# Kernel optimization log

Measured on AMD Instinct MI355X. Metric: run time of the kernel, lower is better.

The kernel has to match this reference:

```python
import jax, jax.numpy as jnp
import numpy as np

N_NODES = 50000
N_EDGES = 500000
D = 128          # n_features
HID = 64         # explainer MLP hidden dim
TEMP = 5.0       # temp[0], epoch-0 temperature
SAMPLE_BIAS = 0.0


def setup_inputs() -> dict:
    key = jax.random.key(0)
    ks = jax.random.split(key, 8)
    embeds = jax.random.normal(ks[0], (N_NODES, D), dtype=jnp.float32)
    W1 = jax.random.normal(ks[1], (3 * D, HID), dtype=jnp.float32) * 0.05
    b1 = jnp.zeros((HID,), dtype=jnp.float32)
    W2 = jax.random.normal(ks[2], (HID, 1), dtype=jnp.float32) * 0.05
    b2 = jnp.zeros((1,), dtype=jnp.float32)
    u = jax.random.uniform(ks[3], (N_EDGES, 1), dtype=jnp.float32)
    src = jax.random.randint(ks[4], (N_EDGES,), 0, N_NODES, dtype=jnp.int64 if jax.config.jax_enable_x64 else jnp.int32)
    dst = jax.random.randint(ks[5], (N_EDGES,), 0, N_NODES, dtype=jnp.int64 if jax.config.jax_enable_x64 else jnp.int32)
    n = 0  # target node index within the subgraph
    return {"embeds": embeds, "W1": W1, "b1": b1, "W2": W2, "b2": b2,
            "u": u, "src": src, "dst": dst, "n": n}


def reference(embeds, W1, b1, W2, b2, u, src, dst, n):
    # --- _create_explainer_input: edge-wise gather + concat with target node embed ---
    row_embeds = embeds[src]                                   # [E, D]
    col_embeds = embeds[dst]                                   # [E, D]
    node_data = jnp.broadcast_to(embeds[n][None, :], row_embeds.shape)  # [E, D]
    inputs = jnp.concatenate([row_embeds, col_embeds, node_data], axis=1)  # [E, 3D]
    # --- explainer_model: Linear(3D,64) -> ReLU -> Linear(64,1) ---
    h = jax.nn.relu(inputs @ W1 + b1)                          # [E, HID]
    sampling_weights = h @ W2 + b2                             # [E, 1]
    # --- _sample_graph (training=True): Gumbel-sigmoid ---
    bias = SAMPLE_BIAS + 0.0001
    eps = (bias - (1.0 - bias)) * u + (1.0 - bias)             # U(bias, 1-bias)
    gate_inputs = jnp.log(eps) - jnp.log1p(-eps)
    mask = jax.nn.sigmoid((gate_inputs + sampling_weights) / TEMP)
    return mask.squeeze(-1)                                    # [E]
```

## Files before the change

### kernel.cpp

```cpp
#include <hip/hip_runtime.h>
#include <hip/hip_bf16.h>


#define D 128
#define HID 64

typedef __attribute__((ext_vector_type(8))) short short8;
typedef __attribute__((ext_vector_type(4))) float f32x4;

__device__ inline unsigned short f2bf(float f) {
    union { float f; unsigned int u; } x;
    x.f = f;
    unsigned int r = x.u + 0x7FFFu + ((x.u >> 16) & 1u);
    return (unsigned short)(r >> 16);
}

__device__ inline unsigned int f2e5u(float f) {
    _Float16 h = (_Float16)f;
    unsigned short u;
    __builtin_memcpy(&u, &h, 2);
    unsigned short r = (unsigned short)(u + 0x7Fu + ((u >> 8) & 1u));
    return (unsigned int)(r >> 8) & 0xFFu;
}
__device__ inline float e5(unsigned short hibits) {
    _Float16 h;
    __builtin_memcpy(&h, &hibits, 2);
    return (float)h;
}

__global__ __launch_bounds__(256) void pg_prep(
    const float* __restrict__ embeds, const float* __restrict__ W1,
    const float* __restrict__ b1, const int* __restrict__ nidx,
    unsigned short* __restrict__ bfrag, float* __restrict__ cnode)
{
    int t = threadIdx.x;
    if (blockIdx.x < 64) {
        int i    = blockIdx.x * 256 + t;
        int j    = i & 7;
        int lane = (i >> 3) & 63;
        int ct   = (i >> 9) & 7;
        int ks   = i >> 12;
        int k    = ks * 32 + (lane >> 4) * 8 + j;
        int col  = ct * 16 + (lane & 15);
        float w  = (col < HID) ? W1[k * HID + col]
                               : W1[(D + k) * HID + (col - HID)];
        bfrag[i] = f2bf(w);
    } else if (t < HID) {
        int n = nidx[0];
        const float* nr = embeds + (size_t)n * D;
        float c = b1[t];
        #pragma unroll 8
        for (int k = 0; k < D; ++k)
            c = fmaf(nr[k], W1[(2 * D + k) * HID + t], c);
        cnode[t] = c;
    }
}

__global__ __launch_bounds__(256) void pg_nodes(
    const float* __restrict__ embeds, const unsigned short* __restrict__ bfrag,
    unsigned char* __restrict__ P, int N, int NTILES)
{
    __shared__ short wl[16384];
    __shared__ unsigned char st[4][16 * 144];
    {
        const uint4* s = reinterpret_cast<const uint4*>(bfrag);
        uint4* d = reinterpret_cast<uint4*>(wl);
        #pragma unroll
        for (int i = 0; i < 8; ++i)
            d[threadIdx.x + i * 256] = s[threadIdx.x + i * 256];
    }
    __syncthreads();

    int wave  = threadIdx.x >> 6;
    int lane  = threadIdx.x & 63;
    int ntile = blockIdx.x * 4 + wave;
    bool active = (ntile < NTILES);

    int kg = lane >> 4;
    if (active) {
        int nr = ntile * 16 + (lane & 15);
        if (nr >= N) nr = N - 1;
        const float* row = embeds + (size_t)nr * D + kg * 8;

        short8 af[4];
        #pragma unroll
        for (int ks = 0; ks < 4; ++ks) {
            float4 v0 = *reinterpret_cast<const float4*>(row + ks * 32);
            float4 v1 = *reinterpret_cast<const float4*>(row + ks * 32 + 4);
            union { float f; unsigned u; } c[8];
            c[0].f = v0.x; c[1].f = v0.y; c[2].f = v0.z; c[3].f = v0.w;
            c[4].f = v1.x; c[5].f = v1.y; c[6].f = v1.z; c[7].f = v1.w;
            union { unsigned u[4]; short8 s; } pk;
            #pragma unroll
            for (int p = 0; p < 4; ++p)
                pk.u[p] = (c[2 * p + 1].u & 0xFFFF0000u) | (c[2 * p].u >> 16);
            af[ks] = pk.s;
        }

        const short8* wl8 = reinterpret_cast<const short8*>(wl);

        f32x4 acc[8];
        #pragma unroll
        for (int ct = 0; ct < 8; ++ct) acc[ct] = (f32x4){0.f, 0.f, 0.f, 0.f};

        #pragma unroll
        for (int ct = 0; ct < 8; ++ct) {
            #pragma unroll
            for (int ks = 0; ks < 4; ++ks) {
                short8 wf = wl8[(ks * 8 + ct) * 64 + lane];
                acc[ct] = __builtin_amdgcn_mfma_f32_16x16x32_bf16(wf, af[ks], acc[ct], 0, 0, 0);
            }
        }

        #pragma unroll
        for (int ct = 0; ct < 8; ++ct) {
            unsigned w = f2e5u(acc[ct][0])
                       | (f2e5u(acc[ct][1]) << 8)
                       | (f2e5u(acc[ct][2]) << 16)
                       | (f2e5u(acc[ct][3]) << 24);
            *reinterpret_cast<unsigned*>(&st[wave][(lane & 15) * 144 + ct * 16 + kg * 4]) = w;
        }
    }
    __syncthreads();

    if (active) {
        #pragma unroll
        for (int h = 0; h < 2; ++h) {
            int c   = lane + h * 64;
            int nr  = c >> 3;
            int off = (c & 7) * 16;
            uint4 v = *reinterpret_cast<const uint4*>(&st[wave][nr * 144 + off]);
            int node = ntile * 16 + nr;
            if (node < N)
                *reinterpret_cast<uint4*>(P + (size_t)node * 128 + off) = v;
        }
    }
}

__global__ __launch_bounds__(256) void pg_edge(
    const unsigned char* __restrict__ P,
    const float* __restrict__ cnode, const float* __restrict__ W2,
    const float* __restrict__ b2, const float* __restrict__ u,
    const int* __restrict__ src, const int* __restrict__ dst,
    float* __restrict__ out, int E)
{
    int e = blockIdx.x * 256 + threadIdx.x;
    if (e >= E) return;

    int se = __builtin_nontemporal_load(src + e);
    int de = __builtin_nontemporal_load(dst + e);
    float uu = __builtin_nontemporal_load(u + e);

    const uint4* ra = reinterpret_cast<const uint4*>(P + (size_t)se * 128);
    const uint4* rb = reinterpret_cast<const uint4*>(P + (size_t)de * 128 + 64);

    uint4 A[4], B[4];
    #pragma unroll
    for (int g = 0; g < 4; ++g) { A[g] = ra[g]; B[g] = rb[g]; }

    float sw = b2[0];
    #pragma unroll
    for (int g = 0; g < 4; ++g) {
        union { uint4 v; unsigned w[4]; } ua, ub;
        ua.v = A[g]; ub.v = B[g];
        #pragma unroll
        for (int w = 0; w < 4; ++w) {
            unsigned wa = ua.w[w], wb = ub.w[w];
            int j = g * 16 + w * 4;
            float h0 = e5((unsigned short)((wa << 8) & 0xFF00u))
                     + e5((unsigned short)((wb << 8) & 0xFF00u)) + cnode[j + 0];
            float h1 = e5((unsigned short)(wa & 0xFF00u))
                     + e5((unsigned short)(wb & 0xFF00u)) + cnode[j + 1];
            float h2 = e5((unsigned short)((wa >> 8) & 0xFF00u))
                     + e5((unsigned short)((wb >> 8) & 0xFF00u)) + cnode[j + 2];
            float h3 = e5((unsigned short)((wa >> 16) & 0xFF00u))
                     + e5((unsigned short)((wb >> 16) & 0xFF00u)) + cnode[j + 3];
            sw = fmaf(fmaxf(h0, 0.f), W2[j + 0], sw);
            sw = fmaf(fmaxf(h1, 0.f), W2[j + 1], sw);
            sw = fmaf(fmaxf(h2, 0.f), W2[j + 2], sw);
            sw = fmaf(fmaxf(h3, 0.f), W2[j + 3], sw);
        }
    }

    float eps = 0.9999f - 0.9998f * uu;
    float gate = logf(eps) - log1pf(-eps);
    float x = (gate + sw) * 0.2f;
    __builtin_nontemporal_store(1.f / (1.f + expf(-x)), out + e);
}

extern "C" void kernel_launch(void* const* d_in, const int* in_sizes, int n_in,
                              void* d_out, int out_size, void* d_ws, size_t ws_size,
                              hipStream_t stream) {
    const float* embeds = (const float*)d_in[0];
    const float* W1     = (const float*)d_in[1];
    const float* b1     = (const float*)d_in[2];
    const float* W2     = (const float*)d_in[3];
    const float* b2     = (const float*)d_in[4];
    const float* u      = (const float*)d_in[5];
    const int*   src    = (const int*)d_in[6];
    const int*   dst    = (const int*)d_in[7];
    const int*   nidx   = (const int*)d_in[8];

    int E = in_sizes[6];
    int N = in_sizes[0] / D;
    int NTILES = (N + 15) / 16;

    unsigned short* bfrag = (unsigned short*)d_ws;
    float* cnode = (float*)(bfrag + 16384);
    unsigned char* P = (unsigned char*)(cnode + 64);

    pg_prep<<<65, 256, 0, stream>>>(embeds, W1, b1, nidx, bfrag, cnode);
    pg_nodes<<<(NTILES + 3) / 4, 256, 0, stream>>>(embeds, bfrag, P, N, NTILES);
    pg_edge<<<(E + 255) / 256, 256, 0, stream>>>(P, cnode, W2, b2, u,
                                                 src, dst, (float*)d_out, E);
}
```

Before: 44.36 us.

## Use packed fp16 math and two edges per thread in edge kernel

The edge kernel now decodes the fp8-like node projections straight into packed half2 pairs, adds bias, applies ReLU and accumulates the second layer with fdot2 in packed fp16. Each thread handles two edges with vectorized index, noise and output accesses, and the gate uses fast log/exp/divide intrinsics. The node kernel reads MFMA weight fragments from global memory instead of staging them in LDS, which drops the block-wide barriers. Half-precision accumulation and fast intrinsics lower accuracy, and the pair layout gives half as many threads for latency hiding.

```diff
diff --git a/kernel.cpp b/kernel.cpp
--- a/kernel.cpp
+++ b/kernel.cpp
@@ -1,5 +1,6 @@
 #include <hip/hip_runtime.h>
 #include <hip/hip_bf16.h>
+#include <string.h>
 
 
 #define D 128
@@ -7,6 +8,9 @@
 
 typedef __attribute__((ext_vector_type(8))) short short8;
 typedef __attribute__((ext_vector_type(4))) float f32x4;
+typedef _Float16 h2 __attribute__((ext_vector_type(2)));
+
+union U32H2 { unsigned u; h2 h; };
 
 __device__ inline unsigned short f2bf(float f) {
     union { float f; unsigned int u; } x;
@@ -22,16 +26,41 @@
     unsigned short r = (unsigned short)(u + 0x7Fu + ((u >> 8) & 1u));
     return (unsigned int)(r >> 8) & 0xFFu;
 }
-__device__ inline float e5(unsigned short hibits) {
-    _Float16 h;
-    __builtin_memcpy(&h, &hibits, 2);
-    return (float)h;
+
+__device__ inline unsigned packh(float lo, float hi) {
+    _Float16 l = (_Float16)lo, h = (_Float16)hi;
+    unsigned short ul, uh;
+    __builtin_memcpy(&ul, &l, 2);
+    __builtin_memcpy(&uh, &h, 2);
+    return (unsigned)ul | ((unsigned)uh << 16);
+}
+
+__device__ inline h2 relu2(h2 x) {
+#if __has_builtin(__builtin_elementwise_max)
+    return __builtin_elementwise_max(x, (h2)((_Float16)0));
+#else
+    h2 r;
+    r[0] = x[0] > (_Float16)0 ? x[0] : (_Float16)0;
+    r[1] = x[1] > (_Float16)0 ? x[1] : (_Float16)0;
+    return r;
+#endif
+}
+
+__device__ inline float dot2acc(h2 a, h2 b, float c) {
+#if __has_builtin(__builtin_amdgcn_fdot2)
+    return __builtin_amdgcn_fdot2(a, b, c, false);
+#else
+    c = fmaf((float)a[0], (float)b[0], c);
+    return fmaf((float)a[1], (float)b[1], c);
+#endif
 }
 
 __global__ __launch_bounds__(256) void pg_prep(
     const float* __restrict__ embeds, const float* __restrict__ W1,
-    const float* __restrict__ b1, const int* __restrict__ nidx,
-    unsigned short* __restrict__ bfrag, float* __restrict__ cnode)
+    const float* __restrict__ b1, const float* __restrict__ W2,
+    const int* __restrict__ nidx,
+    unsigned short* __restrict__ bfrag,
+    unsigned* __restrict__ cnodeh, unsigned* __restrict__ w2h)
 {
     int t = threadIdx.x;
     if (blockIdx.x < 64) {
@@ -45,14 +74,24 @@
         float w  = (col < HID) ? W1[k * HID + col]
                                : W1[(D + k) * HID + (col - HID)];
         bfrag[i] = f2bf(w);
-    } else if (t < HID) {
-        int n = nidx[0];
-        const float* nr = embeds + (size_t)n * D;
-        float c = b1[t];
-        #pragma unroll 8
-        for (int k = 0; k < D; ++k)
-            c = fmaf(nr[k], W1[(2 * D + k) * HID + t], c);
-        cnode[t] = c;
+    } else {
+        __shared__ float cs[HID];
+        if (t < HID) {
+            int n = nidx[0];
+            const float* nr = embeds + (size_t)n * D;
+            float c = b1[t];
+            #pragma unroll 8
+            for (int k = 0; k < D; ++k)
+                c = fmaf(nr[k], W1[(2 * D + k) * HID + t], c);
+            cs[t] = c;
+        }
+        __syncthreads();
+        if (t < 32) {
+            int wi = t >> 1, sub = t & 1;
+            int j = 4 * wi + sub;
+            cnodeh[t] = packh(cs[j], cs[j + 2]);
+            w2h[t]    = packh(W2[j], W2[j + 2]);
+        }
     }
 }
 
@@ -60,132 +99,150 @@
     const float* __restrict__ embeds, const unsigned short* __restrict__ bfrag,
     unsigned char* __restrict__ P, int N, int NTILES)
 {
-    __shared__ short wl[16384];
     __shared__ unsigned char st[4][16 * 144];
-    {
-        const uint4* s = reinterpret_cast<const uint4*>(bfrag);
-        uint4* d = reinterpret_cast<uint4*>(wl);
-        #pragma unroll
-        for (int i = 0; i < 8; ++i)
-            d[threadIdx.x + i * 256] = s[threadIdx.x + i * 256];
-    }
-    __syncthreads();
 
     int wave  = threadIdx.x >> 6;
     int lane  = threadIdx.x & 63;
     int ntile = blockIdx.x * 4 + wave;
-    bool active = (ntile < NTILES);
+    if (ntile >= NTILES) return;
 
     int kg = lane >> 4;
-    if (active) {
-        int nr = ntile * 16 + (lane & 15);
-        if (nr >= N) nr = N - 1;
-        const float* row = embeds + (size_t)nr * D + kg * 8;
-
-        short8 af[4];
+    int nr = ntile * 16 + (lane & 15);
+    if (nr >= N) nr = N - 1;
+    const float* row = embeds + (size_t)nr * D + kg * 8;
+
+    short8 af[4];
+    #pragma unroll
+    for (int ks = 0; ks < 4; ++ks) {
+        float4 v0 = *reinterpret_cast<const float4*>(row + ks * 32);
+        float4 v1 = *reinterpret_cast<const float4*>(row + ks * 32 + 4);
+        union { float f; unsigned u; } c[8];
+        c[0].f = v0.x; c[1].f = v0.y; c[2].f = v0.z; c[3].f = v0.w;
+        c[4].f = v1.x; c[5].f = v1.y; c[6].f = v1.z; c[7].f = v1.w;
+        union { unsigned u[4]; short8 s; } pk;
+        #pragma unroll
+        for (int p = 0; p < 4; ++p)
+            pk.u[p] = (c[2 * p + 1].u & 0xFFFF0000u) | (c[2 * p].u >> 16);
+        af[ks] = pk.s;
+    }
+
+    const short8* gw = reinterpret_cast<const short8*>(bfrag);
+
+    f32x4 acc[8];
+    #pragma unroll
+    for (int ct = 0; ct < 8; ++ct) acc[ct] = (f32x4){0.f, 0.f, 0.f, 0.f};
+
+    #pragma unroll
+    for (int ct = 0; ct < 8; ++ct) {
         #pragma unroll
         for (int ks = 0; ks < 4; ++ks) {
-            float4 v0 = *reinterpret_cast<const float4*>(row + ks * 32);
-            float4 v1 = *reinterpret_cast<const float4*>(row + ks * 32 + 4);
-            union { float f; unsigned u; } c[8];
-            c[0].f = v0.x; c[1].f = v0.y; c[2].f = v0.z; c[3].f = v0.w;
-            c[4].f = v1.x; c[5].f = v1.y; c[6].f = v1.z; c[7].f = v1.w;
-            union { unsigned u[4]; short8 s; } pk;
-            #pragma unroll
-            for (int p = 0; p < 4; ++p)
-                pk.u[p] = (c[2 * p + 1].u & 0xFFFF0000u) | (c[2 * p].u >> 16);
-            af[ks] = pk.s;
-        }
-
-        const short8* wl8 = reinterpret_cast<const short8*>(wl);
-
-        f32x4 acc[8];
+            short8 wf = gw[(ks * 8 + ct) * 64 + lane];
+            acc[ct] = __builtin_amdgcn_mfma_f32_16x16x32_bf16(wf, af[ks], acc[ct], 0, 0, 0);
+        }
+    }
+
+    #pragma unroll
+    for (int ct = 0; ct < 8; ++ct) {
+        unsigned w = f2e5u(acc[ct][0])
+                   | (f2e5u(acc[ct][1]) << 8)
+                   | (f2e5u(acc[ct][2]) << 16)
+                   | (f2e5u(acc[ct][3]) << 24);
+        *reinterpret_cast<unsigned*>(&st[wave][(lane & 15) * 144 + ct * 16 + kg * 4]) = w;
+    }
+    #pragma unroll
+    for (int h = 0; h < 2; ++h) {
+        int c   = lane + h * 64;
+        int r   = c >> 3;
+        int off = (c & 7) * 16;
+        uint4 v = *reinterpret_cast<const uint4*>(&st[wave][r * 144 + off]);
+        int node = ntile * 16 + r;
+        if (node < N)
+            *reinterpret_cast<uint4*>(P + (size_t)node * 128 + off) = v;
+    }
+}
+
+__device__ inline float mlp_sw(const uint4 A[4], const uint4 B[4],
+                               const unsigned* __restrict__ cn,
+                               const unsigned* __restrict__ w2, float sw)
+{
+    #pragma unroll
+    for (int g = 0; g < 4; ++g) {
+        unsigned aw[4] = {A[g].x, A[g].y, A[g].z, A[g].w};
+        unsigned bw[4] = {B[g].x, B[g].y, B[g].z, B[g].w};
         #pragma unroll
-        for (int ct = 0; ct < 8; ++ct) acc[ct] = (f32x4){0.f, 0.f, 0.f, 0.f};
-
-        #pragma unroll
-        for (int ct = 0; ct < 8; ++ct) {
-            #pragma unroll
-            for (int ks = 0; ks < 4; ++ks) {
-                short8 wf = wl8[(ks * 8 + ct) * 64 + lane];
-                acc[ct] = __builtin_amdgcn_mfma_f32_16x16x32_bf16(wf, af[ks], acc[ct], 0, 0, 0);
-            }
-        }
-
-        #pragma unroll
-        for (int ct = 0; ct < 8; ++ct) {
-            unsigned w = f2e5u(acc[ct][0])
-                       | (f2e5u(acc[ct][1]) << 8)
-                       | (f2e5u(acc[ct][2]) << 16)
-                       | (f2e5u(acc[ct][3]) << 24);
-            *reinterpret_cast<unsigned*>(&st[wave][(lane & 15) * 144 + ct * 16 + kg * 4]) = w;
-        }
-    }
-    __syncthreads();
-
-    if (active) {
-        #pragma unroll
-        for (int h = 0; h < 2; ++h) {
-            int c   = lane + h * 64;
-            int nr  = c >> 3;
-            int off = (c & 7) * 16;
-            uint4 v = *reinterpret_cast<const uint4*>(&st[wave][nr * 144 + off]);
-            int node = ntile * 16 + nr;
-            if (node < N)
-                *reinterpret_cast<uint4*>(P + (size_t)node * 128 + off) = v;
-        }
-    }
+        for (int w = 0; w < 4; ++w) {
+            int wi = g * 4 + w;
+            U32H2 a0, a1, b0, b1, c0, c1, W0, W1v;
+            a0.u = (aw[w] << 8) & 0xFF00FF00u;
+            a1.u =  aw[w]       & 0xFF00FF00u;
+            b0.u = (bw[w] << 8) & 0xFF00FF00u;
+            b1.u =  bw[w]       & 0xFF00FF00u;
+            c0.u = cn[2 * wi];     c1.u = cn[2 * wi + 1];
+            W0.u = w2[2 * wi];     W1v.u = w2[2 * wi + 1];
+            h2 h0 = relu2(a0.h + b0.h + c0.h);
+            h2 h1 = relu2(a1.h + b1.h + c1.h);
+            sw = dot2acc(h0, W0.h, sw);
+            sw = dot2acc(h1, W1v.h, sw);
+        }
+    }
+    return sw;
+}
+
+__device__ inline float gumbel_sigmoid(float uu, float sw) {
+    float a = 0.9999f - 0.9998f * uu;
+    float b = 0.0001f + 0.9998f * uu;
+    float gate = __logf(__fdividef(a, b));
+    float x = (gate + sw) * 0.2f;
+    return __fdividef(1.f, 1.f + __expf(-x));
 }
 
 __global__ __launch_bounds__(256) void pg_edge(
     const unsigned char* __restrict__ P,
-    const float* __restrict__ cnode, const float* __restrict__ W2,
+    const unsigned* __restrict__ cnodeh, const unsigned* __restrict__ w2h,
     const float* __restrict__ b2, const float* __restrict__ u,
     const int* __restrict__ src, const int* __restrict__ dst,
     float* __restrict__ out, int E)
 {
-    int e = blockIdx.x * 256 + threadIdx.x;
-    if (e >= E) return;
-
-    int se = __builtin_nontemporal_load(src + e);
-    int de = __builtin_nontemporal_load(dst + e);
-    float uu = __builtin_nontemporal_load(u + e);
-
-    const uint4* ra = reinterpret_cast<const uint4*>(P + (size_t)se * 128);
-    const uint4* rb = reinterpret_cast<const uint4*>(P + (size_t)de * 128 + 64);
-
-    uint4 A[4], B[4];
-    #pragma unroll
-    for (int g = 0; g < 4; ++g) { A[g] = ra[g]; B[g] = rb[g]; }
-
-    float sw = b2[0];
-    #pragma unroll
-    for (int g = 0; g < 4; ++g) {
-        union { uint4 v; unsigned w[4]; } ua, ub;
-        ua.v = A[g]; ub.v = B[g];
-        #pragma unroll
-        for (int w = 0; w < 4; ++w) {
-            unsigned wa = ua.w[w], wb = ub.w[w];
-            int j = g * 16 + w * 4;
-            float h0 = e5((unsigned short)((wa << 8) & 0xFF00u))
-                     + e5((unsigned short)((wb << 8) & 0xFF00u)) + cnode[j + 0];
-            float h1 = e5((unsigned short)(wa & 0xFF00u))
-                     + e5((unsigned short)(wb & 0xFF00u)) + cnode[j + 1];
-            float h2 = e5((unsigned short)((wa >> 8) & 0xFF00u))
-                     + e5((unsigned short)((wb >> 8) & 0xFF00u)) + cnode[j + 2];
-            float h3 = e5((unsigned short)((wa >> 16) & 0xFF00u))
-                     + e5((unsigned short)((wb >> 16) & 0xFF00u)) + cnode[j + 3];
-            sw = fmaf(fmaxf(h0, 0.f), W2[j + 0], sw);
-            sw = fmaf(fmaxf(h1, 0.f), W2[j + 1], sw);
-            sw = fmaf(fmaxf(h2, 0.f), W2[j + 2], sw);
-            sw = fmaf(fmaxf(h3, 0.f), W2[j + 3], sw);
-        }
-    }
-
-    float eps = 0.9999f - 0.9998f * uu;
-    float gate = logf(eps) - log1pf(-eps);
-    float x = (gate + sw) * 0.2f;
-    __builtin_nontemporal_store(1.f / (1.f + expf(-x)), out + e);
+    int p  = blockIdx.x * 256 + threadIdx.x;
+    int e0 = p * 2;
+    if (e0 >= E) return;
+    bool two = (e0 + 1 < E);
+
+    int s0, s1, d0, d1;
+    float u0, u1;
+    if (two) {
+        int2 sv = *reinterpret_cast<const int2*>(src + e0);
+        int2 dv = *reinterpret_cast<const int2*>(dst + e0);
+        float2 uv = *reinterpret_cast<const float2*>(u + e0);
+        s0 = sv.x; s1 = sv.y; d0 = dv.x; d1 = dv.y; u0 = uv.x; u1 = uv.y;
+    } else {
+        s0 = s1 = src[e0]; d0 = d1 = dst[e0]; u0 = u1 = u[e0];
+    }
+
+    const uint4* ra0 = reinterpret_cast<const uint4*>(P + (size_t)s0 * 128);
+    const uint4* rb0 = reinterpret_cast<const uint4*>(P + (size_t)d0 * 128 + 64);
+    const uint4* ra1 = reinterpret_cast<const uint4*>(P + (size_t)s1 * 128);
+    const uint4* rb1 = reinterpret_cast<const uint4*>(P + (size_t)d1 * 128 + 64);
+
+    uint4 A0[4], B0[4], A1[4], B1[4];
+    #pragma unroll
+    for (int g = 0; g < 4; ++g) { A0[g] = ra0[g]; B0[g] = rb0[g]; }
+    #pragma unroll
+    for (int g = 0; g < 4; ++g) { A1[g] = ra1[g]; B1[g] = rb1[g]; }
+
+    float swi = b2[0];
+    float sw0 = mlp_sw(A0, B0, cnodeh, w2h, swi);
+    float sw1 = mlp_sw(A1, B1, cnodeh, w2h, swi);
+
+    float m0 = gumbel_sigmoid(u0, sw0);
+    float m1 = gumbel_sigmoid(u1, sw1);
+
+    if (two) {
+        float2 o = {m0, m1};
+        *reinterpret_cast<float2*>(out + e0) = o;
+    } else {
+        out[e0] = m0;
+    }
 }
 
 extern "C" void kernel_launch(void* const* d_in, const int* in_sizes, int n_in,
@@ -206,11 +263,14 @@
     int NTILES = (N + 15) / 16;
 
     unsigned short* bfrag = (unsigned short*)d_ws;
-    float* cnode = (float*)(bfrag + 16384);
-    unsigned char* P = (unsigned char*)(cnode + 64);
-
-    pg_prep<<<65, 256, 0, stream>>>(embeds, W1, b1, nidx, bfrag, cnode);
+    unsigned* cnodeh = (unsigned*)(bfrag + 16384);
+    unsigned* w2h    = cnodeh + 32;
+    unsigned char* P = (unsigned char*)(w2h + 32);
+
+    pg_prep<<<65, 256, 0, stream>>>(embeds, W1, b1, W2, nidx, bfrag, cnodeh, w2h);
     pg_nodes<<<(NTILES + 3) / 4, 256, 0, stream>>>(embeds, bfrag, P, N, NTILES);
-    pg_edge<<<(E + 255) / 256, 256, 0, stream>>>(P, cnode, W2, b2, u,
-                                                 src, dst, (float*)d_out, E);
-}
+
+    int pairs = (E + 1) / 2;
+    pg_edge<<<(pairs + 255) / 256, 256, 0, stream>>>(P, cnodeh, w2h, b2, u,
+                                                     src, dst, (float*)d_out, E);
+}
```

New measurement: 42.12 us. 5.1% less time.
